# Optimization experiments

Hardware: AMD Instinct MI355X
Metric: run time of the kernel (lower is better)

The kernel has to match this reference:

```python
import jax, jax.numpy as jnp
import numpy as np

N_NODES = 50000
N_EDGES = 800000
D_IN, H, D_OUT = 128, 128, 64


def setup_inputs() -> dict:
    key = jax.random.key(0)
    ks = jax.random.split(key, 8)
    x = jax.random.normal(ks[0], (N_NODES, D_IN), dtype=jnp.float32)
    edge_index = jax.random.randint(ks[1], (2, N_EDGES), 0, N_NODES, dtype=jnp.int64)
    s = 0.05
    return {
        "x": x,
        "edge_index": edge_index,
        # PyG Linear weights are [out, in]; y = x @ W.T + b
        "W_rel1": jax.random.normal(ks[2], (H, D_IN), dtype=jnp.float32) * s,
        "W_root1": jax.random.normal(ks[3], (H, D_IN), dtype=jnp.float32) * s,
        "b1": jax.random.normal(ks[4], (H,), dtype=jnp.float32) * s,
        "W_rel2": jax.random.normal(ks[5], (D_OUT, H), dtype=jnp.float32) * s,
        "W_root2": jax.random.normal(ks[6], (D_OUT, H), dtype=jnp.float32) * s,
        "b2": jax.random.normal(ks[7], (D_OUT,), dtype=jnp.float32) * s,
    }


def graph_conv(x, src, dst, W_rel, W_root, b):
    # sum-aggregate raw neighbor features, then apply linear (equivalent to
    # transforming each message first, but cheaper: one gather + one GEMM).
    agg = jax.ops.segment_sum(x[src], dst, num_segments=N_NODES)  # [N, D]
    return jnp.einsum('nd,hd->nh', agg, W_rel) \
         + jnp.einsum('nd,hd->nh', x, W_root) + b


def reference(x, edge_index, W_rel1, W_root1, b1, W_rel2, W_root2, b2):
    src, dst = edge_index[0], edge_index[1]  # messages flow src -> dst
    t = jax.nn.relu(graph_conv(x, src, dst, W_rel1, W_root1, b1))
    t = graph_conv(t, src, dst, W_rel2, W_root2, b2)
    return t
```

## Files before the change

kernel.cpp:

```cpp
#include <hip/hip_runtime.h>

#define NNODES 50000
#define DIM 128
#define SCAN_CHUNK 4096
#define NSCAN 13
#define PREP_BLOCKS 3200
#define POISON ((int)0xAAAAAAAA)

typedef __attribute__((ext_vector_type(8))) __bf16 bf16x8;
typedef __attribute__((ext_vector_type(4))) float f32x4;

__device__ inline unsigned short f2b(float f) {
    unsigned int u = __float_as_uint(f);
    u += 0x7fffu + ((u >> 16) & 1u);
    return (unsigned short)(u >> 16);
}
__device__ inline float blo(unsigned int u) { return __uint_as_float(u << 16); }
__device__ inline float bhi(unsigned int u) { return __uint_as_float(u & 0xffff0000u); }
__device__ inline unsigned int pack2(float a, float b) {
    return (unsigned int)f2b(a) | ((unsigned int)f2b(b) << 16);
}

__global__ __launch_bounds__(256) void k_prep(
    const float* __restrict__ x, unsigned short* __restrict__ xb, int n4,
    const float* __restrict__ Wa1, const float* __restrict__ Wb1,
    const float* __restrict__ Wa2, const float* __restrict__ Wb2,
    unsigned short* __restrict__ wa1, unsigned short* __restrict__ wb1,
    unsigned short* __restrict__ wa2, unsigned short* __restrict__ wb2,
    const int* __restrict__ dst, int* __restrict__ counts,
    unsigned short* __restrict__ rank, int n_edges)
{
    const int gid = blockIdx.x * 256 + threadIdx.x;

    const int i1 = blockIdx.x * 512 + threadIdx.x;
    const int i2 = i1 + 256;
    const bool ok1 = i1 < n4, ok2 = i2 < n4;
    float4 v1, v2;
    if (ok1) v1 = reinterpret_cast<const float4*>(x)[i1];
    if (ok2) v2 = reinterpret_cast<const float4*>(x)[i2];

    if (gid < n_edges)
        rank[gid] = (unsigned short)(atomicAdd(&counts[dst[gid]], 1) - POISON);

    if (gid < 16384) { wa1[gid] = f2b(Wa1[gid]); wb1[gid] = f2b(Wb1[gid]); }
    if (gid < 8192)  { wa2[gid] = f2b(Wa2[gid]); wb2[gid] = f2b(Wb2[gid]); }

    if (ok1) {
        uint2 o;
        o.x = pack2(v1.x, v1.y);
        o.y = pack2(v1.z, v1.w);
        reinterpret_cast<uint2*>(xb)[i1] = o;
    }
    if (ok2) {
        uint2 o;
        o.x = pack2(v2.x, v2.y);
        o.y = pack2(v2.z, v2.w);
        reinterpret_cast<uint2*>(xb)[i2] = o;
    }
}

__global__ __launch_bounds__(1024) void k_scan_local(
    const int* __restrict__ counts, int* __restrict__ rowptr,
    int* __restrict__ bsum, int n)
{
    __shared__ int wsum[16];
    const int lane = threadIdx.x & 63;
    const int wid = threadIdx.x >> 6;
    int i = blockIdx.x * SCAN_CHUNK + threadIdx.x * 4;
    int4 v = make_int4(0, 0, 0, 0);
    if (i + 3 < n) {
        v = *reinterpret_cast<const int4*>(counts + i);
        v.x -= POISON; v.y -= POISON; v.z -= POISON; v.w -= POISON;
    } else {
        if (i + 0 < n) v.x = counts[i + 0] - POISON;
        if (i + 1 < n) v.y = counts[i + 1] - POISON;
        if (i + 2 < n) v.z = counts[i + 2] - POISON;
    }
    int tot = v.x + v.y + v.z + v.w;
    int s = tot;
#pragma unroll
    for (int off = 1; off < 64; off <<= 1) {
        int t = __shfl_up(s, off);
        if (lane >= off) s += t;
    }
    if (lane == 63) wsum[wid] = s;
    __syncthreads();
    if (wid == 0 && lane < 16) {
        int ws = wsum[lane];
#pragma unroll
        for (int off = 1; off < 16; off <<= 1) {
            int t = __shfl_up(ws, off);
            if (lane >= off) ws += t;
        }
        wsum[lane] = ws;
    }
    __syncthreads();
    int prefix = ((wid > 0) ? wsum[wid - 1] : 0) + (s - tot);
    int4 o;
    o.x = prefix;
    o.y = prefix + v.x;
    o.z = o.y + v.y;
    o.w = o.z + v.z;
    if (i + 3 <= n) {
        *reinterpret_cast<int4*>(rowptr + i) = o;
    } else {
        if (i + 0 <= n) rowptr[i + 0] = o.x;
        if (i + 1 <= n) rowptr[i + 1] = o.y;
        if (i + 2 <= n) rowptr[i + 2] = o.z;
    }
    if (threadIdx.x == 1023) bsum[blockIdx.x] = wsum[15];
}

__device__ inline void build_prefix_lds(const int* __restrict__ bsum, int* pre) {
    if (threadIdx.x < 16) {
        int off = 0;
#pragma unroll 1
        for (int j = 0; j < NSCAN && j < (int)threadIdx.x; ++j) off += bsum[j];
        pre[threadIdx.x] = off;
    }
    __syncthreads();
}

__global__ __launch_bounds__(256) void k_place(
    const int* __restrict__ src, const int* __restrict__ dst,
    const unsigned short* __restrict__ rank, const int* __restrict__ rowptr,
    const int* __restrict__ bsum, unsigned short* __restrict__ srcs_sorted,
    int n_edges)
{
    __shared__ int pre[16];
    build_prefix_lds(bsum, pre);
    int e = (blockIdx.x * 256 + threadIdx.x) * 8;
    if (e + 7 < n_edges) {
        int4 s4a = *reinterpret_cast<const int4*>(src + e);
        int4 s4b = *reinterpret_cast<const int4*>(src + e + 4);
        int4 d4a = *reinterpret_cast<const int4*>(dst + e);
        int4 d4b = *reinterpret_cast<const int4*>(dst + e + 4);
        uint4 r8 = *reinterpret_cast<const uint4*>(rank + e);
        srcs_sorted[rowptr[d4a.x] + pre[d4a.x >> 12] + (int)(r8.x & 0xffffu)] = (unsigned short)s4a.x;
        srcs_sorted[rowptr[d4a.y] + pre[d4a.y >> 12] + (int)(r8.x >> 16)]     = (unsigned short)s4a.y;
        srcs_sorted[rowptr[d4a.z] + pre[d4a.z >> 12] + (int)(r8.y & 0xffffu)] = (unsigned short)s4a.z;
        srcs_sorted[rowptr[d4a.w] + pre[d4a.w >> 12] + (int)(r8.y >> 16)]     = (unsigned short)s4a.w;
        srcs_sorted[rowptr[d4b.x] + pre[d4b.x >> 12] + (int)(r8.z & 0xffffu)] = (unsigned short)s4b.x;
        srcs_sorted[rowptr[d4b.y] + pre[d4b.y >> 12] + (int)(r8.z >> 16)]     = (unsigned short)s4b.y;
        srcs_sorted[rowptr[d4b.z] + pre[d4b.z >> 12] + (int)(r8.w & 0xffffu)] = (unsigned short)s4b.z;
        srcs_sorted[rowptr[d4b.w] + pre[d4b.w >> 12] + (int)(r8.w >> 16)]     = (unsigned short)s4b.w;
    } else {
        for (; e < n_edges; ++e) {
            int d = dst[e];
            srcs_sorted[rowptr[d] + pre[d >> 12] + (int)rank[e]] = (unsigned short)src[e];
        }
    }
}

template <int BN, bool RELU, bool OUTBF16>
__global__ __launch_bounds__(256) void k_fused(
    const unsigned short* __restrict__ F,
    const int* __restrict__ rowptr, const int* __restrict__ bsum,
    const unsigned short* __restrict__ srcs,
    const unsigned short* __restrict__ Wrel,
    const unsigned short* __restrict__ Wroot,
    const float* __restrict__ bias, void* __restrict__ Cout, int n_nodes)
{
    __shared__ int pre[16];
    __shared__ __align__(16) unsigned short agg[32][136];
    build_prefix_lds(bsum, pre);

    const int tid = threadIdx.x;
    const int n0 = blockIdx.x * 32;

#pragma unroll 1
    for (int pass = 0; pass < 2; ++pass) {
        const int nl = pass * 16 + (tid >> 4);
        const int node = n0 + nl;
        const int seg = tid & 15;
        if (node < n_nodes) {
            const int beg = rowptr[node] + pre[node >> 12];
            const int end = rowptr[node + 1] + pre[(node + 1) >> 12];
            float acc[8];
#pragma unroll
            for (int i = 0; i < 8; ++i) acc[i] = 0.f;
            int e = beg;
#pragma unroll 1
            for (; e + 7 < end; e += 8) {
                uint4 v[8];
#pragma unroll
                for (int u = 0; u < 8; ++u) {
                    int s = srcs[e + u];
                    v[u] = *reinterpret_cast<const uint4*>(F + (size_t)s * DIM + seg * 8);
                }
#pragma unroll
                for (int u = 0; u < 8; ++u) {
                    acc[0] += blo(v[u].x); acc[1] += bhi(v[u].x);
                    acc[2] += blo(v[u].y); acc[3] += bhi(v[u].y);
                    acc[4] += blo(v[u].z); acc[5] += bhi(v[u].z);
                    acc[6] += blo(v[u].w); acc[7] += bhi(v[u].w);
                }
            }
#pragma unroll 1
            for (; e + 1 < end; e += 2) {
                int s0 = srcs[e], s1 = srcs[e + 1];
                uint4 v0 = *reinterpret_cast<const uint4*>(F + (size_t)s0 * DIM + seg * 8);
                uint4 v1 = *reinterpret_cast<const uint4*>(F + (size_t)s1 * DIM + seg * 8);
                acc[0] += blo(v0.x) + blo(v1.x); acc[1] += bhi(v0.x) + bhi(v1.x);
                acc[2] += blo(v0.y) + blo(v1.y); acc[3] += bhi(v0.y) + bhi(v1.y);
                acc[4] += blo(v0.z) + blo(v1.z); acc[5] += bhi(v0.z) + bhi(v1.z);
                acc[6] += blo(v0.w) + blo(v1.w); acc[7] += bhi(v0.w) + bhi(v1.w);
            }
            if (e < end) {
                int s0 = srcs[e];
                uint4 v = *reinterpret_cast<const uint4*>(F + (size_t)s0 * DIM + seg * 8);
                acc[0] += blo(v.x); acc[1] += bhi(v.x);
                acc[2] += blo(v.y); acc[3] += bhi(v.y);
                acc[4] += blo(v.z); acc[5] += bhi(v.z);
                acc[6] += blo(v.w); acc[7] += bhi(v.w);
            }
            uint4 o;
            o.x = pack2(acc[0], acc[1]);
            o.y = pack2(acc[2], acc[3]);
            o.z = pack2(acc[4], acc[5]);
            o.w = pack2(acc[6], acc[7]);
            *reinterpret_cast<uint4*>(&agg[nl][seg * 8]) = o;
        }
    }
    __syncthreads();

    constexpr int NT = BN / 32;
    const int wave = tid >> 6;
    const int lane = tid & 63;
    const int quad = lane >> 4;
    const int l16 = lane & 15;
    const int wr = wave >> 1;
    const int wc = wave & 1;
    const int rl = wr * 16 + l16;
    const int grow = n0 + rl;
    const bool ok = grow < n_nodes;

    f32x4 acc[NT];
#pragma unroll
    for (int nt = 0; nt < NT; ++nt) {
        f32x4 z = {0.f, 0.f, 0.f, 0.f};
        acc[nt] = z;
    }

#pragma unroll 1
    for (int kk = 0; kk < 4; ++kk) {
        const int ko = (kk & 1) * 64;
        bf16x8 a0 = {}, a1 = {};
        if (kk < 2) {
            a0 = *reinterpret_cast<const bf16x8*>(&agg[rl][ko + quad * 8]);
            a1 = *reinterpret_cast<const bf16x8*>(&agg[rl][ko + 32 + quad * 8]);
        } else if (ok) {
            a0 = *reinterpret_cast<const bf16x8*>(
                F + (size_t)grow * DIM + ko + quad * 8);
            a1 = *reinterpret_cast<const bf16x8*>(
                F + (size_t)grow * DIM + ko + 32 + quad * 8);
        }
        const unsigned short* __restrict__ W = (kk < 2) ? Wrel : Wroot;
#pragma unroll
        for (int nt = 0; nt < NT; ++nt) {
            bf16x8 b = *reinterpret_cast<const bf16x8*>(
                W + (size_t)(wc * (BN / 2) + nt * 16 + l16) * DIM + ko + quad * 8);
            acc[nt] = __builtin_amdgcn_mfma_f32_16x16x32_bf16(a0, b, acc[nt], 0, 0, 0);
        }
#pragma unroll
        for (int nt = 0; nt < NT; ++nt) {
            bf16x8 b = *reinterpret_cast<const bf16x8*>(
                W + (size_t)(wc * (BN / 2) + nt * 16 + l16) * DIM + ko + 32 + quad * 8);
            acc[nt] = __builtin_amdgcn_mfma_f32_16x16x32_bf16(a1, b, acc[nt], 0, 0, 0);
        }
    }

#pragma unroll
    for (int nt = 0; nt < NT; ++nt) {
        const int col = wc * (BN / 2) + nt * 16 + l16;
        const float bv = bias[col];
#pragma unroll
        for (int reg = 0; reg < 4; ++reg) {
            const int row = n0 + wr * 16 + quad * 4 + reg;
            if (row >= n_nodes) continue;
            float v = acc[nt][reg] + bv;
            if (RELU) v = fmaxf(v, 0.f);
            if (OUTBF16)
                ((unsigned short*)Cout)[(size_t)row * BN + col] = f2b(v);
            else
                ((float*)Cout)[(size_t)row * BN + col] = v;
        }
    }
}

extern "C" void kernel_launch(void* const* d_in, const int* in_sizes, int n_in,
                              void* d_out, int out_size, void* d_ws, size_t ws_size,
                              hipStream_t stream) {
    const float* x       = (const float*)d_in[0];
    const int*   ei      = (const int*)d_in[1];
    const float* W_rel1  = (const float*)d_in[2];
    const float* W_root1 = (const float*)d_in[3];
    const float* b1      = (const float*)d_in[4];
    const float* W_rel2  = (const float*)d_in[5];
    const float* W_root2 = (const float*)d_in[6];
    const float* b2      = (const float*)d_in[7];

    const int n_edges = in_sizes[1] / 2;
    const int* src = ei;
    const int* dst = ei + n_edges;

    const size_t NELEM = (size_t)NNODES * DIM;
    unsigned short* xb   = (unsigned short*)d_ws;
    unsigned short* tb   = xb + NELEM;
    unsigned short* wa1  = tb + NELEM;
    unsigned short* wb1  = wa1 + 16384;
    unsigned short* wa2  = wb1 + 16384;
    unsigned short* wb2  = wa2 + 8192;
    int* counts = (int*)(wb2 + 8192);
    int* rowptr = counts + NNODES;
    int* bsum   = rowptr + (NNODES + 4);
    unsigned short* rank16 = (unsigned short*)(bsum + 20);
    unsigned short* srcs16 = rank16 + n_edges;

    float* out = (float*)d_out;

    const int n4 = NNODES * DIM / 4;
    const int pblocks = (n_edges + 2047) / 2048;
    const int fblocks = (NNODES + 31) / 32;
    const int sblocks = NSCAN;

    k_prep<<<PREP_BLOCKS, 256, 0, stream>>>(
        x, xb, n4, W_rel1, W_root1, W_rel2, W_root2,
        wa1, wb1, wa2, wb2, dst, counts, rank16, n_edges);

    k_scan_local<<<sblocks, 1024, 0, stream>>>(counts, rowptr, bsum, NNODES);
    k_place<<<pblocks, 256, 0, stream>>>(src, dst, rank16, rowptr, bsum, srcs16, n_edges);

    k_fused<128, true, true><<<fblocks, 256, 0, stream>>>(
        xb, rowptr, bsum, srcs16, wa1, wb1, b1, tb, NNODES);

    k_fused<64, false, false><<<fblocks, 256, 0, stream>>>(
        tb, rowptr, bsum, srcs16, wa2, wb2, b2, out, NNODES);
}
```

Before: 256.1 us.

## Transform features before aggregation: split into dual GEMM plus gather-epilogue kernels

Replaces the fused aggregate-then-GEMM kernels with a dual GEMM that computes both X·W_rel^T and X·W_root^T+b per node. A separate gather kernel then sums the transformed neighbor rows and adds the root term, with ReLU for layer 1. For layer 2 this halves the gathered row width (64 vs 128), cutting random-access traffic. The cost is extra intermediate U/R buffers written and re-read, an added kernel launch, and bf16 rounding of the transformed messages before summation. The first dual GEMM is issued before the scan and placement kernels.

```diff
diff --git a/kernel.cpp b/kernel.cpp
--- a/kernel.cpp
+++ b/kernel.cpp
@@ -152,79 +152,18 @@
     }
 }
 
-template <int BN, bool RELU, bool OUTBF16>
-__global__ __launch_bounds__(256) void k_fused(
-    const unsigned short* __restrict__ F,
-    const int* __restrict__ rowptr, const int* __restrict__ bsum,
-    const unsigned short* __restrict__ srcs,
-    const unsigned short* __restrict__ Wrel,
-    const unsigned short* __restrict__ Wroot,
-    const float* __restrict__ bias, void* __restrict__ Cout, int n_nodes)
-{
-    __shared__ int pre[16];
-    __shared__ __align__(16) unsigned short agg[32][136];
-    build_prefix_lds(bsum, pre);
-
+template <int BN>
+__global__ __launch_bounds__(256) void k_gemm_dual(
+    const unsigned short* __restrict__ A,
+    const unsigned short* __restrict__ Wu,
+    const unsigned short* __restrict__ Wr,
+    const float* __restrict__ bias,
+    unsigned short* __restrict__ U,
+    unsigned short* __restrict__ R,
+    int n_nodes)
+{
+    constexpr int NT = BN / 32;
     const int tid = threadIdx.x;
-    const int n0 = blockIdx.x * 32;
-
-#pragma unroll 1
-    for (int pass = 0; pass < 2; ++pass) {
-        const int nl = pass * 16 + (tid >> 4);
-        const int node = n0 + nl;
-        const int seg = tid & 15;
-        if (node < n_nodes) {
-            const int beg = rowptr[node] + pre[node >> 12];
-            const int end = rowptr[node + 1] + pre[(node + 1) >> 12];
-            float acc[8];
-#pragma unroll
-            for (int i = 0; i < 8; ++i) acc[i] = 0.f;
-            int e = beg;
-#pragma unroll 1
-            for (; e + 7 < end; e += 8) {
-                uint4 v[8];
-#pragma unroll
-                for (int u = 0; u < 8; ++u) {
-                    int s = srcs[e + u];
-                    v[u] = *reinterpret_cast<const uint4*>(F + (size_t)s * DIM + seg * 8);
-                }
-#pragma unroll
-                for (int u = 0; u < 8; ++u) {
-                    acc[0] += blo(v[u].x); acc[1] += bhi(v[u].x);
-                    acc[2] += blo(v[u].y); acc[3] += bhi(v[u].y);
-                    acc[4] += blo(v[u].z); acc[5] += bhi(v[u].z);
-                    acc[6] += blo(v[u].w); acc[7] += bhi(v[u].w);
-                }
-            }
-#pragma unroll 1
-            for (; e + 1 < end; e += 2) {
-                int s0 = srcs[e], s1 = srcs[e + 1];
-                uint4 v0 = *reinterpret_cast<const uint4*>(F + (size_t)s0 * DIM + seg * 8);
-                uint4 v1 = *reinterpret_cast<const uint4*>(F + (size_t)s1 * DIM + seg * 8);
-                acc[0] += blo(v0.x) + blo(v1.x); acc[1] += bhi(v0.x) + bhi(v1.x);
-                acc[2] += blo(v0.y) + blo(v1.y); acc[3] += bhi(v0.y) + bhi(v1.y);
-                acc[4] += blo(v0.z) + blo(v1.z); acc[5] += bhi(v0.z) + bhi(v1.z);
-                acc[6] += blo(v0.w) + blo(v1.w); acc[7] += bhi(v0.w) + bhi(v1.w);
-            }
-            if (e < end) {
-                int s0 = srcs[e];
-                uint4 v = *reinterpret_cast<const uint4*>(F + (size_t)s0 * DIM + seg * 8);
-                acc[0] += blo(v.x); acc[1] += bhi(v.x);
-                acc[2] += blo(v.y); acc[3] += bhi(v.y);
-                acc[4] += blo(v.z); acc[5] += bhi(v.z);
-                acc[6] += blo(v.w); acc[7] += bhi(v.w);
-            }
-            uint4 o;
-            o.x = pack2(acc[0], acc[1]);
-            o.y = pack2(acc[2], acc[3]);
-            o.z = pack2(acc[4], acc[5]);
-            o.w = pack2(acc[6], acc[7]);
-            *reinterpret_cast<uint4*>(&agg[nl][seg * 8]) = o;
-        }
-    }
-    __syncthreads();
-
-    constexpr int NT = BN / 32;
     const int wave = tid >> 6;
     const int lane = tid & 63;
     const int quad = lane >> 4;
@@ -232,41 +171,37 @@
     const int wr = wave >> 1;
     const int wc = wave & 1;
     const int rl = wr * 16 + l16;
-    const int grow = n0 + rl;
-    const bool ok = grow < n_nodes;
-
-    f32x4 acc[NT];
+    const int n0 = blockIdx.x * 32;
+    const int arow = n0 + rl;
+    const bool ok = arow < n_nodes;
+
+    f32x4 accU[NT], accR[NT];
 #pragma unroll
     for (int nt = 0; nt < NT; ++nt) {
         f32x4 z = {0.f, 0.f, 0.f, 0.f};
-        acc[nt] = z;
-    }
-
-#pragma unroll 1
-    for (int kk = 0; kk < 4; ++kk) {
-        const int ko = (kk & 1) * 64;
+        accU[nt] = z;
+        accR[nt] = z;
+    }
+
+#pragma unroll 1
+    for (int kk = 0; kk < 2; ++kk) {
+        const int ko = kk * 64;
         bf16x8 a0 = {}, a1 = {};
-        if (kk < 2) {
-            a0 = *reinterpret_cast<const bf16x8*>(&agg[rl][ko + quad * 8]);
-            a1 = *reinterpret_cast<const bf16x8*>(&agg[rl][ko + 32 + quad * 8]);
-        } else if (ok) {
-            a0 = *reinterpret_cast<const bf16x8*>(
-                F + (size_t)grow * DIM + ko + quad * 8);
-            a1 = *reinterpret_cast<const bf16x8*>(
-                F + (size_t)grow * DIM + ko + 32 + quad * 8);
-        }
-        const unsigned short* __restrict__ W = (kk < 2) ? Wrel : Wroot;
+        if (ok) {
+            a0 = *reinterpret_cast<const bf16x8*>(A + (size_t)arow * DIM + ko + quad * 8);
+            a1 = *reinterpret_cast<const bf16x8*>(A + (size_t)arow * DIM + ko + 32 + quad * 8);
+        }
 #pragma unroll
         for (int nt = 0; nt < NT; ++nt) {
-            bf16x8 b = *reinterpret_cast<const bf16x8*>(
-                W + (size_t)(wc * (BN / 2) + nt * 16 + l16) * DIM + ko + quad * 8);
-            acc[nt] = __builtin_amdgcn_mfma_f32_16x16x32_bf16(a0, b, acc[nt], 0, 0, 0);
-        }
-#pragma unroll
-        for (int nt = 0; nt < NT; ++nt) {
-            bf16x8 b = *reinterpret_cast<const bf16x8*>(
-                W + (size_t)(wc * (BN / 2) + nt * 16 + l16) * DIM + ko + 32 + quad * 8);
-            acc[nt] = __builtin_amdgcn_mfma_f32_16x16x32_bf16(a1, b, acc[nt], 0, 0, 0);
+            const size_t woff = (size_t)(wc * (BN / 2) + nt * 16 + l16) * DIM + ko + quad * 8;
+            bf16x8 bu0 = *reinterpret_cast<const bf16x8*>(Wu + woff);
+            bf16x8 br0 = *reinterpret_cast<const bf16x8*>(Wr + woff);
+            accU[nt] = __builtin_amdgcn_mfma_f32_16x16x32_bf16(a0, bu0, accU[nt], 0, 0, 0);
+            accR[nt] = __builtin_amdgcn_mfma_f32_16x16x32_bf16(a0, br0, accR[nt], 0, 0, 0);
+            bf16x8 bu1 = *reinterpret_cast<const bf16x8*>(Wu + woff + 32);
+            bf16x8 br1 = *reinterpret_cast<const bf16x8*>(Wr + woff + 32);
+            accU[nt] = __builtin_amdgcn_mfma_f32_16x16x32_bf16(a1, bu1, accU[nt], 0, 0, 0);
+            accR[nt] = __builtin_amdgcn_mfma_f32_16x16x32_bf16(a1, br1, accR[nt], 0, 0, 0);
         }
     }
 
@@ -278,14 +213,137 @@
         for (int reg = 0; reg < 4; ++reg) {
             const int row = n0 + wr * 16 + quad * 4 + reg;
             if (row >= n_nodes) continue;
-            float v = acc[nt][reg] + bv;
-            if (RELU) v = fmaxf(v, 0.f);
-            if (OUTBF16)
-                ((unsigned short*)Cout)[(size_t)row * BN + col] = f2b(v);
-            else
-                ((float*)Cout)[(size_t)row * BN + col] = v;
-        }
-    }
+            U[(size_t)row * BN + col] = f2b(accU[nt][reg]);
+            R[(size_t)row * BN + col] = f2b(accR[nt][reg] + bv);
+        }
+    }
+}
+
+__global__ __launch_bounds__(256) void k_gather_ep1(
+    const unsigned short* __restrict__ U, const unsigned short* __restrict__ R,
+    const int* __restrict__ rowptr, const int* __restrict__ bsum,
+    const unsigned short* __restrict__ srcs, unsigned short* __restrict__ T)
+{
+    __shared__ int pre[16];
+    build_prefix_lds(bsum, pre);
+    int node = blockIdx.x * 16 + (threadIdx.x >> 4);
+    if (node >= NNODES) return;
+    int seg = threadIdx.x & 15;
+    int beg = rowptr[node] + pre[node >> 12];
+    int end = rowptr[node + 1] + pre[(node + 1) >> 12];
+    float acc[8];
+#pragma unroll
+    for (int i = 0; i < 8; ++i) acc[i] = 0.f;
+    int e = beg;
+#pragma unroll 1
+    for (; e + 7 < end; e += 8) {
+        uint4 v[8];
+#pragma unroll
+        for (int u = 0; u < 8; ++u) {
+            int s = srcs[e + u];
+            v[u] = *reinterpret_cast<const uint4*>(U + (size_t)s * DIM + seg * 8);
+        }
+#pragma unroll
+        for (int u = 0; u < 8; ++u) {
+            acc[0] += blo(v[u].x); acc[1] += bhi(v[u].x);
+            acc[2] += blo(v[u].y); acc[3] += bhi(v[u].y);
+            acc[4] += blo(v[u].z); acc[5] += bhi(v[u].z);
+            acc[6] += blo(v[u].w); acc[7] += bhi(v[u].w);
+        }
+    }
+#pragma unroll 1
+    for (; e + 1 < end; e += 2) {
+        int s0 = srcs[e], s1 = srcs[e + 1];
+        uint4 v0 = *reinterpret_cast<const uint4*>(U + (size_t)s0 * DIM + seg * 8);
+        uint4 v1 = *reinterpret_cast<const uint4*>(U + (size_t)s1 * DIM + seg * 8);
+        acc[0] += blo(v0.x) + blo(v1.x); acc[1] += bhi(v0.x) + bhi(v1.x);
+        acc[2] += blo(v0.y) + blo(v1.y); acc[3] += bhi(v0.y) + bhi(v1.y);
+        acc[4] += blo(v0.z) + blo(v1.z); acc[5] += bhi(v0.z) + bhi(v1.z);
+        acc[6] += blo(v0.w) + blo(v1.w); acc[7] += bhi(v0.w) + bhi(v1.w);
+    }
+    if (e < end) {
+        int s0 = srcs[e];
+        uint4 v = *reinterpret_cast<const uint4*>(U + (size_t)s0 * DIM + seg * 8);
+        acc[0] += blo(v.x); acc[1] += bhi(v.x);
+        acc[2] += blo(v.y); acc[3] += bhi(v.y);
+        acc[4] += blo(v.z); acc[5] += bhi(v.z);
+        acc[6] += blo(v.w); acc[7] += bhi(v.w);
+    }
+    uint4 rv = *reinterpret_cast<const uint4*>(R + (size_t)node * DIM + seg * 8);
+    acc[0] += blo(rv.x); acc[1] += bhi(rv.x);
+    acc[2] += blo(rv.y); acc[3] += bhi(rv.y);
+    acc[4] += blo(rv.z); acc[5] += bhi(rv.z);
+    acc[6] += blo(rv.w); acc[7] += bhi(rv.w);
+#pragma unroll
+    for (int i = 0; i < 8; ++i) acc[i] = fmaxf(acc[i], 0.f);
+    uint4 o;
+    o.x = pack2(acc[0], acc[1]);
+    o.y = pack2(acc[2], acc[3]);
+    o.z = pack2(acc[4], acc[5]);
+    o.w = pack2(acc[6], acc[7]);
+    *reinterpret_cast<uint4*>(T + (size_t)node * DIM + seg * 8) = o;
+}
+
+__global__ __launch_bounds__(256) void k_gather_ep2(
+    const unsigned short* __restrict__ U, const unsigned short* __restrict__ R,
+    const int* __restrict__ rowptr, const int* __restrict__ bsum,
+    const unsigned short* __restrict__ srcs, float* __restrict__ out)
+{
+    __shared__ int pre[16];
+    build_prefix_lds(bsum, pre);
+    int node = blockIdx.x * 32 + (threadIdx.x >> 3);
+    if (node >= NNODES) return;
+    int seg = threadIdx.x & 7;
+    int beg = rowptr[node] + pre[node >> 12];
+    int end = rowptr[node + 1] + pre[(node + 1) >> 12];
+    float acc[8];
+#pragma unroll
+    for (int i = 0; i < 8; ++i) acc[i] = 0.f;
+    int e = beg;
+#pragma unroll 1
+    for (; e + 7 < end; e += 8) {
+        uint4 v[8];
+#pragma unroll
+        for (int u = 0; u < 8; ++u) {
+            int s = srcs[e + u];
+            v[u] = *reinterpret_cast<const uint4*>(U + (size_t)s * 64 + seg * 8);
+        }
+#pragma unroll
+        for (int u = 0; u < 8; ++u) {
+            acc[0] += blo(v[u].x); acc[1] += bhi(v[u].x);
+            acc[2] += blo(v[u].y); acc[3] += bhi(v[u].y);
+            acc[4] += blo(v[u].z); acc[5] += bhi(v[u].z);
+            acc[6] += blo(v[u].w); acc[7] += bhi(v[u].w);
+        }
+    }
+#pragma unroll 1
+    for (; e + 1 < end; e += 2) {
+        int s0 = srcs[e], s1 = srcs[e + 1];
+        uint4 v0 = *reinterpret_cast<const uint4*>(U + (size_t)s0 * 64 + seg * 8);
+        uint4 v1 = *reinterpret_cast<const uint4*>(U + (size_t)s1 * 64 + seg * 8);
+        acc[0] += blo(v0.x) + blo(v1.x); acc[1] += bhi(v0.x) + bhi(v1.x);
+        acc[2] += blo(v0.y) + blo(v1.y); acc[3] += bhi(v0.y) + bhi(v1.y);
+        acc[4] += blo(v0.z) + blo(v1.z); acc[5] += bhi(v0.z) + bhi(v1.z);
+        acc[6] += blo(v0.w) + blo(v1.w); acc[7] += bhi(v0.w) + bhi(v1.w);
+    }
+    if (e < end) {
+        int s0 = srcs[e];
+        uint4 v = *reinterpret_cast<const uint4*>(U + (size_t)s0 * 64 + seg * 8);
+        acc[0] += blo(v.x); acc[1] += bhi(v.x);
+        acc[2] += blo(v.y); acc[3] += bhi(v.y);
+        acc[4] += blo(v.z); acc[5] += bhi(v.z);
+        acc[6] += blo(v.w); acc[7] += bhi(v.w);
+    }
+    uint4 rv = *reinterpret_cast<const uint4*>(R + (size_t)node * 64 + seg * 8);
+    acc[0] += blo(rv.x); acc[1] += bhi(rv.x);
+    acc[2] += blo(rv.y); acc[3] += bhi(rv.y);
+    acc[4] += blo(rv.z); acc[5] += bhi(rv.z);
+    acc[6] += blo(rv.w); acc[7] += bhi(rv.w);
+    float4 o0 = make_float4(acc[0], acc[1], acc[2], acc[3]);
+    float4 o1 = make_float4(acc[4], acc[5], acc[6], acc[7]);
+    float* op = out + (size_t)node * 64 + seg * 8;
+    *reinterpret_cast<float4*>(op) = o0;
+    *reinterpret_cast<float4*>(op + 4) = o1;
 }
 
 extern "C" void kernel_launch(void* const* d_in, const int* in_sizes, int n_in,
@@ -307,7 +365,11 @@
     const size_t NELEM = (size_t)NNODES * DIM;
     unsigned short* xb   = (unsigned short*)d_ws;
     unsigned short* tb   = xb + NELEM;
-    unsigned short* wa1  = tb + NELEM;
+    unsigned short* u1   = tb + NELEM;
+    unsigned short* r1   = u1 + NELEM;
+    unsigned short* u2   = r1 + NELEM;
+    unsigned short* r2   = u2 + (size_t)NNODES * 64;
+    unsigned short* wa1  = r2 + (size_t)NNODES * 64;
     unsigned short* wb1  = wa1 + 16384;
     unsigned short* wa2  = wb1 + 16384;
     unsigned short* wb2  = wa2 + 8192;
@@ -321,19 +383,24 @@
 
     const int n4 = NNODES * DIM / 4;
     const int pblocks = (n_edges + 2047) / 2048;
-    const int fblocks = (NNODES + 31) / 32;
+    const int g1blocks = (NNODES + 15) / 16;
+    const int g2blocks = (NNODES + 31) / 32;
+    const int gemm_blocks = (NNODES + 31) / 32;
     const int sblocks = NSCAN;
 
     k_prep<<<PREP_BLOCKS, 256, 0, stream>>>(
         x, xb, n4, W_rel1, W_root1, W_rel2, W_root2,
         wa1, wb1, wa2, wb2, dst, counts, rank16, n_edges);
 
+    k_gemm_dual<128><<<gemm_blocks, 256, 0, stream>>>(
+        xb, wa1, wb1, b1, u1, r1, NNODES);
+
     k_scan_local<<<sblocks, 1024, 0, stream>>>(counts, rowptr, bsum, NNODES);
     k_place<<<pblocks, 256, 0, stream>>>(src, dst, rank16, rowptr, bsum, srcs16, n_edges);
 
-    k_fused<128, true, true><<<fblocks, 256, 0, stream>>>(
-        xb, rowptr, bsum, srcs16, wa1, wb1, b1, tb, NNODES);
-
-    k_fused<64, false, false><<<fblocks, 256, 0, stream>>>(
-        tb, rowptr, bsum, srcs16, wa2, wb2, b2, out, NNODES);
-}
+    k_gather_ep1<<<g1blocks, 256, 0, stream>>>(u1, r1, rowptr, bsum, srcs16, tb);
+
+    k_gemm_dual<64><<<gemm_blocks, 256, 0, stream>>>(
+        tb, wa2, wb2, b2, u2, r2, NNODES);
+    k_gather_ep2<<<g2blocks, 256, 0, stream>>>(u2, r2, rowptr, bsum, srcs16, out);
+}
```

Result: faster. 245.8 us (-4.0%).
